# Performance work log

Measured on AMD Instinct MI355X. Metric: run time of the kernel, lower is better.

The kernel has to match this reference:

```python
import jax, jax.numpy as jnp
import numpy as np

HEADS = 16
DIM_HEAD = 64
SCALE = DIM_HEAD ** -0.5


def setup_inputs() -> dict:
    key = jax.random.key(0)
    k1, k2, k3, k4 = jax.random.split(key, 4)
    b, n, dim = 4, 4096, 1024
    dim_inner = HEADS * DIM_HEAD
    x = jax.random.normal(k1, (b, n, dim), dtype=jnp.float32)
    W_qkv = jax.random.normal(k2, (dim, dim_inner * 3), dtype=jnp.float32) * 0.02
    agent_tokens = jax.random.normal(k3, (HEADS, 128, DIM_HEAD), dtype=jnp.float32) * 0.02
    W_out = jax.random.normal(k4, (dim_inner, dim), dtype=jnp.float32) * 0.02
    return {"x": x, "W_qkv": W_qkv, "agent_tokens": agent_tokens, "W_out": W_out}


def reference(x, W_qkv, agent_tokens, W_out):
    b, n, _ = x.shape
    h, m, d = agent_tokens.shape
    # qkv projection: b n (3 h d) -> 3, b, h, n, d
    qkv = (x @ W_qkv).reshape(b, n, 3, h, d).transpose(2, 0, 3, 1, 4)
    q, k, v = qkv[0], qkv[1], qkv[2]
    a = agent_tokens * SCALE  # h m d, broadcast over batch
    qa_sim = jnp.einsum('bhid,hjd->bhij', q, a)   # b h n m
    ak_sim = jnp.einsum('hid,bhjd->bhij', a, k)   # b h m n
    qa_attn = jax.nn.softmax(qa_sim, axis=-1)
    ak_attn = jax.nn.softmax(ak_sim, axis=-1)
    out = jnp.einsum('bhij,bhjd->bhid', ak_attn, v)    # b h m d
    out = jnp.einsum('bhij,bhjd->bhid', qa_attn, out)  # b h n d
    out = out.transpose(0, 2, 1, 3).reshape(b, n, h * d)
    return out @ W_out
```

## Files before the change

### kernel.cpp

```cpp
#include <hip/hip_runtime.h>

typedef __bf16 bf16x8 __attribute__((ext_vector_type(8)));
typedef float f32x4 __attribute__((ext_vector_type(4)));
typedef unsigned short ushort8 __attribute__((ext_vector_type(8)));
typedef unsigned short u16;

#define MFMA16(a, b, c) __builtin_amdgcn_mfma_f32_16x16x32_bf16(a, b, c, 0, 0, 0)
#define FENCE() __builtin_amdgcn_sched_barrier(0)
#define BARRIER() do { FENCE(); __builtin_amdgcn_s_barrier(); FENCE(); } while (0)
#define VMCNT(n) do { FENCE(); asm volatile("s_waitcnt vmcnt(" #n ")"); FENCE(); } while (0)

__device__ __forceinline__ u16 f2bf(float v) {
  unsigned int u = __builtin_bit_cast(unsigned int, v);
  u += 0x7fffu + ((u >> 16) & 1u);
  return (u16)(u >> 16);
}

__device__ __forceinline__ void gload16(const u16* g, u16* l) {
  __builtin_amdgcn_global_load_lds((__attribute__((address_space(1))) void*)(g),
                                   (__attribute__((address_space(3))) void*)(l), 16, 0, 0);
}

__global__ __launch_bounds__(256) void prep(const float* __restrict__ x, u16* __restrict__ x_bf,
                                            const float* __restrict__ Wqkv, u16* __restrict__ wqkvT,
                                            const float* __restrict__ Wout, u16* __restrict__ woutT,
                                            const float* __restrict__ agent, u16* __restrict__ a_bf) {
  __shared__ float tile[64][65];
  int bid = blockIdx.x;
  int t = threadIdx.x;
  if (bid < 8192) {
    size_t i = (size_t)bid * 256 + t;
    const float4* p = (const float4*)x + i * 2;
    float4 a = p[0], b = p[1];
    ushort8 o;
    o[0] = f2bf(a.x); o[1] = f2bf(a.y); o[2] = f2bf(a.z); o[3] = f2bf(a.w);
    o[4] = f2bf(b.x); o[5] = f2bf(b.y); o[6] = f2bf(b.z); o[7] = f2bf(b.w);
    *((ushort8*)x_bf + i) = o;
    return;
  }
  if (bid >= 9216) {
    int i = (bid - 9216) * 256 + t;
    a_bf[i] = f2bf(agent[i] * 0.125f);
    return;
  }
  const float* W; u16* WT; int K = 1024, N; int b2;
  if (bid < 8960) { W = Wqkv; WT = wqkvT; N = 3072; b2 = bid - 8192; }
  else            { W = Wout; WT = woutT; N = 1024; b2 = bid - 8960; }
  int nt = N >> 6;
  int kt = b2 / nt, nti = b2 - kt * nt;
  int k0 = kt << 6, n0 = nti << 6;
  int r = t >> 4, c4 = (t & 15) << 2;
#pragma unroll
  for (int j = 0; j < 4; ++j) {
    float4 v = *(const float4*)&W[(size_t)(k0 + j * 16 + r) * N + n0 + c4];
    tile[j * 16 + r][c4] = v.x; tile[j * 16 + r][c4 + 1] = v.y;
    tile[j * 16 + r][c4 + 2] = v.z; tile[j * 16 + r][c4 + 3] = v.w;
  }
  __syncthreads();
  int rn = t >> 2, cs = (t & 3) << 4;
  ushort8 o0, o1;
#pragma unroll
  for (int e = 0; e < 8; ++e) { o0[e] = f2bf(tile[cs + e][rn]); o1[e] = f2bf(tile[cs + 8 + e][rn]); }
  u16* dst = WT + (size_t)(n0 + rn) * K + k0 + cs;
  *(ushort8*)dst = o0;
  *(ushort8*)(dst + 8) = o1;
}

template <int MODE>
__global__ __launch_bounds__(512, 2) void gemm256(const u16* __restrict__ A, const u16* __restrict__ BT,
                                                  int M, int N, int K,
                                                  u16* __restrict__ qb, u16* __restrict__ kb,
                                                  u16* __restrict__ vt, float* __restrict__ outf) {
  extern __shared__ char smem[];
  const int NT = K >> 5;
  int ntiles = N >> 8;
  int nwg = (M >> 8) * ntiles;
  int bid = blockIdx.x;
  int wg = (bid & 7) * (nwg >> 3) + (bid >> 3);
  int tm = wg / ntiles, tn = wg - tm * ntiles;
  int rb = tm << 8, cb = tn << 8;
  int t = threadIdx.x;
  int w = t >> 6, lane = t & 63, li = lane & 15, lg = lane >> 4;
  int wr = w >> 2, wc = w & 3;

  const u16* srcA[2];
  const u16* srcB[2];
#pragma unroll
  for (int j = 0; j < 2; ++j) {
    int D = j * 8192 + t * 16;
    int L = D ^ (((D >> 7) & 3) << 4);
    int row = L >> 6, inb = L & 63;
    srcA[j] = A + (size_t)(rb + row) * K + (inb >> 1);
    srcB[j] = BT + (size_t)(cb + row) * K + (inb >> 1);
  }
#define STAGE_A(slot, kt) do { \
    gload16(srcA[0] + (kt) * 32, (u16*)(smem + (slot) * 32768 + t * 16)); \
    gload16(srcA[1] + (kt) * 32, (u16*)(smem + (slot) * 32768 + 8192 + t * 16)); } while (0)
#define STAGE_B(slot, kt) do { \
    gload16(srcB[0] + (kt) * 32, (u16*)(smem + (slot) * 32768 + 16384 + t * 16)); \
    gload16(srcB[1] + (kt) * 32, (u16*)(smem + (slot) * 32768 + 24576 + t * 16)); } while (0)

  int offA[8], offB[4];
#pragma unroll
  for (int m8 = 0; m8 < 8; ++m8) {
    int row = wr * 128 + m8 * 16 + li;
    int L = row * 64 + lg * 16;
    offA[m8] = L ^ (((L >> 7) & 3) << 4);
  }
#pragma unroll
  for (int n = 0; n < 4; ++n) {
    int row = wc * 64 + n * 16 + li;
    int L = row * 64 + lg * 16;
    offB[n] = 16384 + (L ^ (((L >> 7) & 3) << 4));
  }

  f32x4 acc[8][4];
#pragma unroll
  for (int m = 0; m < 8; ++m)
#pragma unroll
    for (int n = 0; n < 4; ++n) acc[m][n] = (f32x4){0.f, 0.f, 0.f, 0.f};

  bf16x8 aF[4], aS[4], bfr[4];

#define RD_A_LO(sb, d) do { d[0] = *(const bf16x8*)((sb) + offA[0]); d[1] = *(const bf16x8*)((sb) + offA[1]); \
                            d[2] = *(const bf16x8*)((sb) + offA[2]); d[3] = *(const bf16x8*)((sb) + offA[3]); } while (0)
#define RD_A_HI(sb, d) do { d[0] = *(const bf16x8*)((sb) + offA[4]); d[1] = *(const bf16x8*)((sb) + offA[5]); \
                            d[2] = *(const bf16x8*)((sb) + offA[6]); d[3] = *(const bf16x8*)((sb) + offA[7]); } while (0)
#define RD_B(sb, d)    do { d[0] = *(const bf16x8*)((sb) + offB[0]); d[1] = *(const bf16x8*)((sb) + offB[1]); \
                            d[2] = *(const bf16x8*)((sb) + offB[2]); d[3] = *(const bf16x8*)((sb) + offB[3]); } while (0)

#define GBODY(tt, STG, WAITOP) do { \
    char* sb_ = smem + ((tt) & 3) * 32768; \
    if (STG) { STAGE_A(((tt) + 3) & 3, (tt) + 3); STAGE_B(((tt) + 3) & 3, (tt) + 3); } \
    RD_B(sb_, bfr); RD_A_LO(sb_, aF); RD_A_HI(sb_, aS); \
    _Pragma("unroll") for (int m = 0; m < 4; ++m) \
      _Pragma("unroll") for (int n = 0; n < 4; ++n) acc[m][n] = MFMA16(aF[m], bfr[n], acc[m][n]); \
    _Pragma("unroll") for (int m = 0; m < 4; ++m) \
      _Pragma("unroll") for (int n = 0; n < 4; ++n) acc[4 + m][n] = MFMA16(aS[m], bfr[n], acc[4 + m][n]); \
    WAITOP; \
    __builtin_amdgcn_s_barrier(); \
    FENCE(); \
  } while (0)

  STAGE_A(0, 0); STAGE_B(0, 0);
  STAGE_A(1, 1); STAGE_B(1, 1);
  STAGE_A(2, 2); STAGE_B(2, 2);
  VMCNT(8);
  __builtin_amdgcn_s_barrier();
  FENCE();

  for (int tt = 0; tt < NT - 3; ++tt) GBODY(tt, 1, VMCNT(8));
  GBODY(NT - 3, 0, VMCNT(4));
  GBODY(NT - 2, 0, VMCNT(0));
  GBODY(NT - 1, 0, ((void)0));

  if (MODE == 0) {
    int col0 = cb + wc * 64;
    int s = col0 >> 10;
    int hh = (col0 >> 6) & 15;
    if (s < 2) {
      u16* dst = (s == 0) ? qb : kb;
#pragma unroll
      for (int m = 0; m < 8; ++m) {
        int rbase = rb + wr * 128 + m * 16 + lg * 4;
#pragma unroll
        for (int r = 0; r < 4; ++r) {
          int rr = rbase + r;
          size_t o = (((size_t)(rr >> 12) * 16 + hh) * 4096 + (rr & 4095)) * 64;
#pragma unroll
          for (int n = 0; n < 4; ++n) dst[o + n * 16 + li] = f2bf(acc[m][n][r]);
        }
      }
    } else {
      BARRIER();
#pragma unroll
      for (int m = 0; m < 8; ++m) {
        int rl = wr * 128 + m * 16 + lg * 4;
#pragma unroll
        for (int n = 0; n < 4; ++n) {
          int colL = wc * 64 + n * 16 + li;
          unsigned int lo = (unsigned int)f2bf(acc[m][n][0]) | ((unsigned int)f2bf(acc[m][n][1]) << 16);
          unsigned int hi = (unsigned int)f2bf(acc[m][n][2]) | ((unsigned int)f2bf(acc[m][n][3]) << 16);
          int byte = (colL * 512 + rl * 2) ^ ((colL & 7) << 4);
          *(uint2*)(smem + byte) = make_uint2(lo, hi);
        }
      }
      BARRIER();
      int bb = rb >> 12, nnb = rb & 4095;
      int hh0b = (cb >> 6) & 15;
#pragma unroll
      for (int it = 0; it < 16; ++it) {
        int c = (it & 3) * 64 + w * 8 + (lane >> 3);
        int k = (it >> 2) * 8 + (lane & 7);
        int kk = (k & ~7) | ((k & 7) ^ (c & 7));
        uint4 v = *(const uint4*)(smem + c * 512 + kk * 16);
        size_t off = (((size_t)bb * 16 + hh0b + (c >> 6)) * 64 + (c & 63)) * 4096 + nnb + k * 8;
        *(uint4*)(vt + off) = v;
      }
    }
  } else {
#pragma unroll
    for (int m = 0; m < 8; ++m) {
#pragma unroll
      for (int r = 0; r < 4; ++r) {
        float* po = outf + (size_t)(rb + wr * 128 + m * 16 + lg * 4 + r) * N + cb + wc * 64;
#pragma unroll
        for (int n = 0; n < 4; ++n) po[n * 16 + li] = acc[m][n][r];
      }
    }
  }
#undef GBODY
#undef RD_A_LO
#undef RD_A_HI
#undef RD_B
#undef STAGE_A
#undef STAGE_B
}

__global__ __launch_bounds__(256) void ak_flash(const u16* __restrict__ kb, const u16* __restrict__ vt,
                                                const u16* __restrict__ ab,
                                                float* __restrict__ pO, float* __restrict__ pM,
                                                float* __restrict__ pL) {
  __shared__ u16 p_lds[128][136];
  int bid = blockIdx.x;
  int s = bid & 7;
  int bh = bid >> 3;
  int h = bh & 15;
  int t = threadIdx.x, w = t >> 6, l = t & 63, lg = l >> 4, li = l & 15;
  int jb = w * 32;

  bf16x8 afr[2][2];
#pragma unroll
  for (int jt = 0; jt < 2; ++jt)
#pragma unroll
    for (int kk = 0; kk < 2; ++kk)
      afr[jt][kk] = *(const bf16x8*)&ab[(size_t)(h * 128 + jb + jt * 16 + li) * 64 + kk * 32 + lg * 8];

  f32x4 O[2][4];
  float mrow[2][4], lrow[2][4];
#pragma unroll
  for (int jt = 0; jt < 2; ++jt) {
#pragma unroll
    for (int dt = 0; dt < 4; ++dt) O[jt][dt] = (f32x4){0.f, 0.f, 0.f, 0.f};
#pragma unroll
    for (int r = 0; r < 4; ++r) { mrow[jt][r] = -1e30f; lrow[jt][r] = 0.f; }
  }
  const u16* kbase = kb + (size_t)bh * 4096 * 64;
  const u16* vbase = vt + (size_t)bh * 64 * 4096;

  for (int c = 0; c < 4; ++c) {
    int i0 = s * 512 + c * 128;
    f32x4 sf[2][8];
#pragma unroll
    for (int jt = 0; jt < 2; ++jt)
#pragma unroll
      for (int it = 0; it < 8; ++it) sf[jt][it] = (f32x4){0.f, 0.f, 0.f, 0.f};
#pragma unroll
    for (int it = 0; it < 8; ++it)
#pragma unroll
      for (int kk = 0; kk < 2; ++kk) {
        bf16x8 bfr = *(const bf16x8*)&kbase[(size_t)(i0 + it * 16 + li) * 64 + kk * 32 + lg * 8];
        sf[0][it] = MFMA16(afr[0][kk], bfr, sf[0][it]);
        sf[1][it] = MFMA16(afr[1][kk], bfr, sf[1][it]);
      }
#pragma unroll
    for (int jt = 0; jt < 2; ++jt)
#pragma unroll
      for (int r = 0; r < 4; ++r) {
        float cm = sf[jt][0][r];
#pragma unroll
        for (int it = 1; it < 8; ++it) cm = fmaxf(cm, sf[jt][it][r]);
#pragma unroll
        for (int off = 1; off < 16; off <<= 1) cm = fmaxf(cm, __shfl_xor(cm, off));
        float mold = mrow[jt][r];
        float mnew = fmaxf(mold, cm);
        float scale = __expf(mold - mnew);
        float ss = 0.f;
#pragma unroll
        for (int it = 0; it < 8; ++it) {
          float p = __expf(sf[jt][it][r] - mnew);
          sf[jt][it][r] = p;
          ss += p;
        }
#pragma unroll
        for (int off = 1; off < 16; off <<= 1) ss += __shfl_xor(ss, off);
        lrow[jt][r] = lrow[jt][r] * scale + ss;
        mrow[jt][r] = mnew;
#pragma unroll
        for (int dt = 0; dt < 4; ++dt) O[jt][dt][r] *= scale;
      }
#pragma unroll
    for (int jt = 0; jt < 2; ++jt)
#pragma unroll
      for (int it = 0; it < 8; ++it)
#pragma unroll
        for (int r = 0; r < 4; ++r)
          p_lds[jb + jt * 16 + lg * 4 + r][it * 16 + li] = f2bf(sf[jt][it][r]);
#pragma unroll
    for (int ks = 0; ks < 4; ++ks) {
      bf16x8 pa0 = *(const bf16x8*)&p_lds[jb + li][ks * 32 + lg * 8];
      bf16x8 pa1 = *(const bf16x8*)&p_lds[jb + 16 + li][ks * 32 + lg * 8];
#pragma unroll
      for (int dt = 0; dt < 4; ++dt) {
        bf16x8 bv = *(const bf16x8*)&vbase[(size_t)(dt * 16 + li) * 4096 + i0 + ks * 32 + lg * 8];
        O[0][dt] = MFMA16(pa0, bv, O[0][dt]);
        O[1][dt] = MFMA16(pa1, bv, O[1][dt]);
      }
    }
  }
  size_t pb = ((size_t)bh * 8 + s) * 128;
#pragma unroll
  for (int jt = 0; jt < 2; ++jt)
#pragma unroll
    for (int dt = 0; dt < 4; ++dt)
#pragma unroll
      for (int r = 0; r < 4; ++r) {
        int j = jb + jt * 16 + lg * 4 + r;
        pO[(pb + j) * 64 + dt * 16 + li] = O[jt][dt][r];
      }
  if (li == 0) {
#pragma unroll
    for (int jt = 0; jt < 2; ++jt)
#pragma unroll
      for (int r = 0; r < 4; ++r) {
        int j = jb + jt * 16 + lg * 4 + r;
        pM[pb + j] = mrow[jt][r];
        pL[pb + j] = lrow[jt][r];
      }
  }
}

__global__ __launch_bounds__(128) void ak_combine(const float* __restrict__ pO, const float* __restrict__ pM,
                                                  const float* __restrict__ pL, u16* __restrict__ out1t) {
  int bh = blockIdx.x >> 3, dc = blockIdx.x & 7;
  int j = threadIdx.x;
  float ms[8], wv[8];
  float M = -1e30f;
#pragma unroll
  for (int s = 0; s < 8; ++s) { ms[s] = pM[((size_t)bh * 8 + s) * 128 + j]; M = fmaxf(M, ms[s]); }
  float L = 0.f;
#pragma unroll
  for (int s = 0; s < 8; ++s) { wv[s] = __expf(ms[s] - M); L += wv[s] * pL[((size_t)bh * 8 + s) * 128 + j]; }
  float inv = 1.f / L;
  float4 A = {0.f, 0.f, 0.f, 0.f}, B = {0.f, 0.f, 0.f, 0.f};
#pragma unroll
  for (int s = 0; s < 8; ++s) {
    const float4* p = (const float4*)&pO[(((size_t)bh * 8 + s) * 128 + j) * 64 + dc * 8];
    float4 x = p[0], y = p[1];
    A.x += wv[s] * x.x; A.y += wv[s] * x.y; A.z += wv[s] * x.z; A.w += wv[s] * x.w;
    B.x += wv[s] * y.x; B.y += wv[s] * y.y; B.z += wv[s] * y.z; B.w += wv[s] * y.w;
  }
  size_t ob = ((size_t)bh * 64 + dc * 8) * 128 + j;
  out1t[ob + 0 * 128] = f2bf(A.x * inv);
  out1t[ob + 1 * 128] = f2bf(A.y * inv);
  out1t[ob + 2 * 128] = f2bf(A.z * inv);
  out1t[ob + 3 * 128] = f2bf(A.w * inv);
  out1t[ob + 4 * 128] = f2bf(B.x * inv);
  out1t[ob + 5 * 128] = f2bf(B.y * inv);
  out1t[ob + 6 * 128] = f2bf(B.z * inv);
  out1t[ob + 7 * 128] = f2bf(B.w * inv);
}

__global__ __launch_bounds__(256) void qa_fused(const u16* __restrict__ qb, const u16* __restrict__ out1t,
                                                const u16* __restrict__ ab, u16* __restrict__ out2) {
  __shared__ u16 p_lds[128][136];
  int bid = blockIdx.x;
  int nt = bid & 31;
  int bh = bid >> 5;
  int h = bh & 15, b = bh >> 4;
  int t = threadIdx.x, w = t >> 6, l = t & 63, lg = l >> 4, li = l & 15;
  int n0 = nt * 128;

  const u16* qbase = qb + ((size_t)bh * 4096 + n0 + w * 32) * 64;
  bf16x8 qf[2][2];
#pragma unroll
  for (int rt = 0; rt < 2; ++rt)
#pragma unroll
    for (int kk = 0; kk < 2; ++kk)
      qf[rt][kk] = *(const bf16x8*)&qbase[(size_t)(rt * 16 + li) * 64 + kk * 32 + lg * 8];

  f32x4 sf[2][8];
#pragma unroll
  for (int rt = 0; rt < 2; ++rt)
#pragma unroll
    for (int jt = 0; jt < 8; ++jt) sf[rt][jt] = (f32x4){0.f, 0.f, 0.f, 0.f};

  const u16* abase = ab + h * 128 * 64;
#pragma unroll
  for (int jt = 0; jt < 8; ++jt)
#pragma unroll
    for (int kk = 0; kk < 2; ++kk) {
      bf16x8 bfr = *(const bf16x8*)&abase[(size_t)(jt * 16 + li) * 64 + kk * 32 + lg * 8];
      sf[0][jt] = MFMA16(qf[0][kk], bfr, sf[0][jt]);
      sf[1][jt] = MFMA16(qf[1][kk], bfr, sf[1][jt]);
    }
  float inv[2][4];
#pragma unroll
  for (int rt = 0; rt < 2; ++rt)
#pragma unroll
    for (int r = 0; r < 4; ++r) {
      float cm = sf[rt][0][r];
#pragma unroll
      for (int jt = 1; jt < 8; ++jt) cm = fmaxf(cm, sf[rt][jt][r]);
#pragma unroll
      for (int off = 1; off < 16; off <<= 1) cm = fmaxf(cm, __shfl_xor(cm, off));
      float ss = 0.f;
#pragma unroll
      for (int jt = 0; jt < 8; ++jt) {
        float p = __expf(sf[rt][jt][r] - cm);
        sf[rt][jt][r] = p;
        ss += p;
      }
#pragma unroll
      for (int off = 1; off < 16; off <<= 1) ss += __shfl_xor(ss, off);
      inv[rt][r] = 1.f / ss;
    }
#pragma unroll
  for (int rt = 0; rt < 2; ++rt)
#pragma unroll
    for (int jt = 0; jt < 8; ++jt)
#pragma unroll
      for (int r = 0; r < 4; ++r)
        p_lds[w * 32 + rt * 16 + lg * 4 + r][jt * 16 + li] = f2bf(sf[rt][jt][r]);

  f32x4 O[2][4];
#pragma unroll
  for (int rt = 0; rt < 2; ++rt)
#pragma unroll
    for (int dt = 0; dt < 4; ++dt) O[rt][dt] = (f32x4){0.f, 0.f, 0.f, 0.f};

  const u16* obase = out1t + (size_t)bh * 64 * 128;
#pragma unroll
  for (int ks = 0; ks < 4; ++ks) {
    bf16x8 pa0 = *(const bf16x8*)&p_lds[w * 32 + li][ks * 32 + lg * 8];
    bf16x8 pa1 = *(const bf16x8*)&p_lds[w * 32 + 16 + li][ks * 32 + lg * 8];
#pragma unroll
    for (int dt = 0; dt < 4; ++dt) {
      bf16x8 bv = *(const bf16x8*)&obase[(size_t)(dt * 16 + li) * 128 + ks * 32 + lg * 8];
      O[0][dt] = MFMA16(pa0, bv, O[0][dt]);
      O[1][dt] = MFMA16(pa1, bv, O[1][dt]);
    }
  }
#pragma unroll
  for (int rt = 0; rt < 2; ++rt)
#pragma unroll
    for (int dt = 0; dt < 4; ++dt)
#pragma unroll
      for (int r = 0; r < 4; ++r) {
        int nn = n0 + w * 32 + rt * 16 + lg * 4 + r;
        int col = h * 64 + dt * 16 + li;
        out2[((size_t)b * 4096 + nn) * 1024 + col] = f2bf(O[rt][dt][r] * inv[rt][r]);
      }
}

extern "C" void kernel_launch(void* const* d_in, const int* in_sizes, int n_in,
                              void* d_out, int out_size, void* d_ws, size_t ws_size,
                              hipStream_t stream) {
  const float* x = (const float*)d_in[0];
  const float* Wqkv = (const float*)d_in[1];
  const float* agent = (const float*)d_in[2];
  const float* Wout = (const float*)d_in[3];
  float* out = (float*)d_out;

  char* ws = (char*)d_ws;
  u16* x_bf  = (u16*)(ws + 0);
  u16* wqkvT = (u16*)(ws + 33554432);
  u16* woutT = (u16*)(ws + 39845888);
  u16* a_bf  = (u16*)(ws + 41943040);
  u16* qb    = (u16*)(ws + 42205184);
  u16* kb    = (u16*)(ws + 75759616);
  u16* vt    = (u16*)(ws + 142868480);
  float* pO  = (float*)(ws + 176422912);
  float* pM  = (float*)(ws + 193200128);
  float* pL  = (float*)(ws + 193724416);
  u16* out1t = (u16*)(ws + 194248704);
  u16* out2  = x_bf;

  (void)hipFuncSetAttribute((const void*)gemm256<0>, hipFuncAttributeMaxDynamicSharedMemorySize, 131072);
  (void)hipFuncSetAttribute((const void*)gemm256<1>, hipFuncAttributeMaxDynamicSharedMemorySize, 131072);

  prep<<<9728, 256, 0, stream>>>(x, x_bf, Wqkv, wqkvT, Wout, woutT, agent, a_bf);
  gemm256<0><<<768, 512, 131072, stream>>>(x_bf, wqkvT, 16384, 3072, 1024, qb, kb, vt, nullptr);
  ak_flash<<<512, 256, 0, stream>>>(kb, vt, a_bf, pO, pM, pL);
  ak_combine<<<512, 128, 0, stream>>>(pO, pM, pL, out1t);
  qa_fused<<<2048, 256, 0, stream>>>(qb, out1t, a_bf, out2);
  gemm256<1><<<256, 512, 131072, stream>>>(out2, woutT, 16384, 1024, 1024, nullptr, nullptr, nullptr, out);
}
```

Baseline: 285.7 us.

## Restructure GEMM main loop into 64-wide K tiles with phased ping-pong scheduling

Changes the 256x256 GEMM mainloop from a 4-slot, 32-wide K ring buffer to a 2-slot double buffer with 64-wide K tiles and a new XOR swizzle. Each tile is split into four phases separated by barriers, where LDS fragment reads and next-tile global loads are interleaved with MFMA bursts run at raised priority via s_setprio. The aim is to cut per-tile barrier/wait overhead and overlap memory with compute the way ping-pong schedules do. In exchange the prefetch depth drops to one tile, there are more barriers per tile, and the mainloop waits for all outstanding loads (vmcnt 0) every tile.

```diff
diff --git a/kernel.cpp b/kernel.cpp
--- a/kernel.cpp
+++ b/kernel.cpp
@@ -9,6 +9,7 @@
 #define FENCE() __builtin_amdgcn_sched_barrier(0)
 #define BARRIER() do { FENCE(); __builtin_amdgcn_s_barrier(); FENCE(); } while (0)
 #define VMCNT(n) do { FENCE(); asm volatile("s_waitcnt vmcnt(" #n ")"); FENCE(); } while (0)
+#define LGKM0() do { asm volatile("s_waitcnt lgkmcnt(0)"); FENCE(); } while (0)
 
 __device__ __forceinline__ u16 f2bf(float v) {
   unsigned int u = __builtin_bit_cast(unsigned int, v);
@@ -72,7 +73,7 @@
                                                   u16* __restrict__ qb, u16* __restrict__ kb,
                                                   u16* __restrict__ vt, float* __restrict__ outf) {
   extern __shared__ char smem[];
-  const int NT = K >> 5;
+  const int NT = K >> 6;
   int ntiles = N >> 8;
   int nwg = (M >> 8) * ntiles;
   int bid = blockIdx.x;
@@ -82,37 +83,34 @@
   int t = threadIdx.x;
   int w = t >> 6, lane = t & 63, li = lane & 15, lg = lane >> 4;
   int wr = w >> 2, wc = w & 3;
-
-  const u16* srcA[2];
-  const u16* srcB[2];
-#pragma unroll
-  for (int j = 0; j < 2; ++j) {
-    int D = j * 8192 + t * 16;
-    int L = D ^ (((D >> 7) & 3) << 4);
-    int row = L >> 6, inb = L & 63;
-    srcA[j] = A + (size_t)(rb + row) * K + (inb >> 1);
-    srcB[j] = BT + (size_t)(cb + row) * K + (inb >> 1);
-  }
-#define STAGE_A(slot, kt) do { \
-    gload16(srcA[0] + (kt) * 32, (u16*)(smem + (slot) * 32768 + t * 16)); \
-    gload16(srcA[1] + (kt) * 32, (u16*)(smem + (slot) * 32768 + 8192 + t * 16)); } while (0)
-#define STAGE_B(slot, kt) do { \
-    gload16(srcB[0] + (kt) * 32, (u16*)(smem + (slot) * 32768 + 16384 + t * 16)); \
-    gload16(srcB[1] + (kt) * 32, (u16*)(smem + (slot) * 32768 + 24576 + t * 16)); } while (0)
+  int swz = li & 7;
+
+  const u16* srcA[2][2];
+  const u16* srcB[2][2];
+#pragma unroll
+  for (int h = 0; h < 2; ++h)
+#pragma unroll
+    for (int i = 0; i < 2; ++i) {
+      int D = t * 16 + i * 8192;
+      int drow = D >> 7, dc16 = (D >> 4) & 7;
+      int lc = (dc16 ^ (drow & 7)) * 8;
+      srcA[h][i] = A + (size_t)(rb + h * 128 + drow) * K + lc;
+      srcB[h][i] = BT + (size_t)(cb + h * 128 + drow) * K + lc;
+    }
+#define STAGE_H(r, TT) do { \
+    char* db_ = smem + ((TT) & 1) * 65536 + (r) * 16384; \
+    const u16* s0_ = ((r) < 2 ? srcA[(r) & 1][0] : srcB[(r) & 1][0]) + ((TT) << 6); \
+    const u16* s1_ = ((r) < 2 ? srcA[(r) & 1][1] : srcB[(r) & 1][1]) + ((TT) << 6); \
+    gload16(s0_, (u16*)(db_ + t * 16)); \
+    gload16(s1_, (u16*)(db_ + 8192 + t * 16)); } while (0)
 
   int offA[8], offB[4];
 #pragma unroll
-  for (int m8 = 0; m8 < 8; ++m8) {
-    int row = wr * 128 + m8 * 16 + li;
-    int L = row * 64 + lg * 16;
-    offA[m8] = L ^ (((L >> 7) & 3) << 4);
-  }
-#pragma unroll
-  for (int n = 0; n < 4; ++n) {
-    int row = wc * 64 + n * 16 + li;
-    int L = row * 64 + lg * 16;
-    offB[n] = 16384 + (L ^ (((L >> 7) & 3) << 4));
-  }
+  for (int m = 0; m < 8; ++m)
+    offA[m] = wr * 16384 + (m * 16 + li) * 128 + ((lg ^ swz) << 4);
+#pragma unroll
+  for (int n = 0; n < 4; ++n)
+    offB[n] = 32768 + (wc >> 1) * 16384 + ((wc & 1) * 64 + n * 16 + li) * 128 + ((lg ^ swz) << 4);
 
   f32x4 acc[8][4];
 #pragma unroll
@@ -120,39 +118,60 @@
 #pragma unroll
     for (int n = 0; n < 4; ++n) acc[m][n] = (f32x4){0.f, 0.f, 0.f, 0.f};
 
-  bf16x8 aF[4], aS[4], bfr[4];
-
-#define RD_A_LO(sb, d) do { d[0] = *(const bf16x8*)((sb) + offA[0]); d[1] = *(const bf16x8*)((sb) + offA[1]); \
-                            d[2] = *(const bf16x8*)((sb) + offA[2]); d[3] = *(const bf16x8*)((sb) + offA[3]); } while (0)
-#define RD_A_HI(sb, d) do { d[0] = *(const bf16x8*)((sb) + offA[4]); d[1] = *(const bf16x8*)((sb) + offA[5]); \
-                            d[2] = *(const bf16x8*)((sb) + offA[6]); d[3] = *(const bf16x8*)((sb) + offA[7]); } while (0)
-#define RD_B(sb, d)    do { d[0] = *(const bf16x8*)((sb) + offB[0]); d[1] = *(const bf16x8*)((sb) + offB[1]); \
-                            d[2] = *(const bf16x8*)((sb) + offB[2]); d[3] = *(const bf16x8*)((sb) + offB[3]); } while (0)
-
-#define GBODY(tt, STG, WAITOP) do { \
-    char* sb_ = smem + ((tt) & 3) * 32768; \
-    if (STG) { STAGE_A(((tt) + 3) & 3, (tt) + 3); STAGE_B(((tt) + 3) & 3, (tt) + 3); } \
-    RD_B(sb_, bfr); RD_A_LO(sb_, aF); RD_A_HI(sb_, aS); \
+  bf16x8 aA[4][2], bA[2][2], bB[2][2];
+#define LDV(off) (*(const bf16x8*)(sb_ + (off)))
+
+#define PH_TAIL() do { \
+    FENCE(); __builtin_amdgcn_s_barrier(); LGKM0(); \
+    __builtin_amdgcn_s_setprio(1); } while (0)
+#define PH_END() do { \
+    __builtin_amdgcn_s_setprio(0); \
+    FENCE(); __builtin_amdgcn_s_barrier(); FENCE(); } while (0)
+
+#define TILE64(TT, STG, WAITOP) do { \
+    char* sb_ = smem + ((TT) & 1) * 65536; \
+     \
+    _Pragma("unroll") for (int m = 0; m < 4; ++m) { aA[m][0] = LDV(offA[m]); aA[m][1] = LDV(offA[m] ^ 64); } \
+    _Pragma("unroll") for (int n = 0; n < 2; ++n) { bA[n][0] = LDV(offB[n]); bA[n][1] = LDV(offB[n] ^ 64); } \
+    if (STG) { STAGE_H(0, (TT) + 1); STAGE_H(1, (TT) + 1); } \
+    PH_TAIL(); \
     _Pragma("unroll") for (int m = 0; m < 4; ++m) \
-      _Pragma("unroll") for (int n = 0; n < 4; ++n) acc[m][n] = MFMA16(aF[m], bfr[n], acc[m][n]); \
+      _Pragma("unroll") for (int n = 0; n < 2; ++n) \
+        _Pragma("unroll") for (int k2 = 0; k2 < 2; ++k2) acc[m][n] = MFMA16(aA[m][k2], bA[n][k2], acc[m][n]); \
+    PH_END(); \
+     \
+    _Pragma("unroll") for (int n = 0; n < 2; ++n) { bB[n][0] = LDV(offB[2 + n]); bB[n][1] = LDV(offB[2 + n] ^ 64); } \
+    if (STG) { STAGE_H(2, (TT) + 1); STAGE_H(3, (TT) + 1); } \
+    PH_TAIL(); \
     _Pragma("unroll") for (int m = 0; m < 4; ++m) \
-      _Pragma("unroll") for (int n = 0; n < 4; ++n) acc[4 + m][n] = MFMA16(aS[m], bfr[n], acc[4 + m][n]); \
+      _Pragma("unroll") for (int n = 0; n < 2; ++n) \
+        _Pragma("unroll") for (int k2 = 0; k2 < 2; ++k2) acc[m][2 + n] = MFMA16(aA[m][k2], bB[n][k2], acc[m][2 + n]); \
+    PH_END(); \
+     \
+    _Pragma("unroll") for (int m = 0; m < 4; ++m) { aA[m][0] = LDV(offA[4 + m]); aA[m][1] = LDV(offA[4 + m] ^ 64); } \
+    _Pragma("unroll") for (int n = 0; n < 2; ++n) { bA[n][0] = LDV(offB[n]); bA[n][1] = LDV(offB[n] ^ 64); } \
+    PH_TAIL(); \
+    _Pragma("unroll") for (int m = 0; m < 4; ++m) \
+      _Pragma("unroll") for (int n = 0; n < 2; ++n) \
+        _Pragma("unroll") for (int k2 = 0; k2 < 2; ++k2) acc[4 + m][n] = MFMA16(aA[m][k2], bA[n][k2], acc[4 + m][n]); \
+    PH_END(); \
+     \
+    _Pragma("unroll") for (int n = 0; n < 2; ++n) { bB[n][0] = LDV(offB[2 + n]); bB[n][1] = LDV(offB[2 + n] ^ 64); } \
+    PH_TAIL(); \
+    _Pragma("unroll") for (int m = 0; m < 4; ++m) \
+      _Pragma("unroll") for (int n = 0; n < 2; ++n) \
+        _Pragma("unroll") for (int k2 = 0; k2 < 2; ++k2) acc[4 + m][2 + n] = MFMA16(aA[m][k2], bB[n][k2], acc[4 + m][2 + n]); \
+    __builtin_amdgcn_s_setprio(0); \
     WAITOP; \
-    __builtin_amdgcn_s_barrier(); \
-    FENCE(); \
+    FENCE(); __builtin_amdgcn_s_barrier(); FENCE(); \
   } while (0)
 
-  STAGE_A(0, 0); STAGE_B(0, 0);
-  STAGE_A(1, 1); STAGE_B(1, 1);
-  STAGE_A(2, 2); STAGE_B(2, 2);
-  VMCNT(8);
-  __builtin_amdgcn_s_barrier();
-  FENCE();
-
-  for (int tt = 0; tt < NT - 3; ++tt) GBODY(tt, 1, VMCNT(8));
-  GBODY(NT - 3, 0, VMCNT(4));
-  GBODY(NT - 2, 0, VMCNT(0));
-  GBODY(NT - 1, 0, ((void)0));
+  STAGE_H(0, 0); STAGE_H(1, 0); STAGE_H(2, 0); STAGE_H(3, 0);
+  VMCNT(0);
+  BARRIER();
+
+  for (int TT = 0; TT < NT - 1; ++TT) TILE64(TT, 1, VMCNT(0));
+  TILE64(NT - 1, 0, ((void)0));
 
   if (MODE == 0) {
     int col0 = cb + wc * 64;
@@ -209,12 +228,11 @@
       }
     }
   }
-#undef GBODY
-#undef RD_A_LO
-#undef RD_A_HI
-#undef RD_B
-#undef STAGE_A
-#undef STAGE_B
+#undef TILE64
+#undef PH_TAIL
+#undef PH_END
+#undef LDV
+#undef STAGE_H
 }
 
 __global__ __launch_bounds__(256) void ak_flash(const u16* __restrict__ kb, const u16* __restrict__ vt,
```

Result: faster. 279.1 us (-2.3%).
